# Kernel tuning notes

Hardware: AMD Instinct MI355X
Metric: run time of the kernel (lower is better)

The kernel has to match this reference:

```python
import jax, jax.numpy as jnp
import numpy as np

NUM_HEADS = 12
SEQ_H = 32
SEQ_W = 32
D_HALF = 32
ROPE_BASE = 10000.0
LN_EPS = 1e-5


def build_rope_cache(seq_len, head_dim, base=ROPE_BASE):
    inv_freq = 1.0 / base ** (jnp.arange(0, head_dim, 2, dtype=jnp.float32) / head_dim)
    t = jnp.arange(seq_len, dtype=jnp.float32)
    freqs = jnp.outer(t, inv_freq)  # [seq_len, head_dim//2]
    cos = jnp.repeat(jnp.cos(freqs), 2, axis=-1)  # [seq_len, head_dim]
    sin = jnp.repeat(jnp.sin(freqs), 2, axis=-1)
    return cos, sin


def apply_rope(x, cos, sin):
    # x: [B,H,N,d_sub], cos/sin: [N,d_sub]
    x_even, x_odd = x[..., ::2], x[..., 1::2]
    x_rot = jnp.stack([-x_odd, x_even], axis=-1).reshape(x.shape)
    return x * cos[None, None] + x_rot * sin[None, None]


def setup_inputs() -> dict:
    key = jax.random.key(0)
    ks = jax.random.split(key, 3)
    B, N, D = 8, 1025, 768
    return {
        "x": jax.random.normal(ks[0], (B, N, D), dtype=jnp.float32),
        "ln_g": jnp.ones((D,), dtype=jnp.float32),
        "ln_b": jnp.zeros((D,), dtype=jnp.float32),
        "w_qkv": jax.random.normal(ks[1], (3 * D, D), dtype=jnp.float32) * 0.02,
        "w_proj": jax.random.normal(ks[2], (D, D), dtype=jnp.float32) * 0.02,
        "b_proj": jnp.zeros((D,), dtype=jnp.float32),
    }


def reference(x, ln_g, ln_b, w_qkv, w_proj, b_proj):
    B, N, D = x.shape
    H = NUM_HEADS
    hd = D // H
    d2 = D_HALF
    scale = hd ** -0.5

    # LayerNorm
    mu = jnp.mean(x, axis=-1, keepdims=True)
    var = jnp.mean(jnp.square(x - mu), axis=-1, keepdims=True)
    xn = (x - mu) * jax.lax.rsqrt(var + LN_EPS) * ln_g + ln_b

    # QKV projection (no bias)
    qkv = jnp.einsum("bnd,ed->bne", xn, w_qkv).reshape(B, N, 3, H, hd)
    qkv = jnp.transpose(qkv, (2, 0, 3, 1, 4))  # [3,B,H,N,hd]
    q, k, v = qkv[0], qkv[1], qkv[2]

    # 2D position ids (CLS token -> row 0, col 0)
    patch_lin = jnp.arange(N - 1)
    rows = patch_lin // SEQ_W
    cols = patch_lin % SEQ_W
    zero = jnp.zeros((1,), dtype=patch_lin.dtype)
    row_ids = jnp.concatenate([zero, rows])
    col_ids = jnp.concatenate([zero, cols])

    cos_row, sin_row = build_rope_cache(SEQ_H, d2)
    cos_col, sin_col = build_rope_cache(SEQ_W, d2)
    cos_r, sin_r = cos_row[row_ids], sin_row[row_ids]  # [N,d2]
    cos_c, sin_c = cos_col[col_ids], sin_col[col_ids]

    q = jnp.concatenate(
        [apply_rope(q[..., :d2], cos_r, sin_r), apply_rope(q[..., d2:], cos_c, sin_c)], axis=-1)
    k = jnp.concatenate(
        [apply_rope(k[..., :d2], cos_r, sin_r), apply_rope(k[..., d2:], cos_c, sin_c)], axis=-1)

    attn = jnp.einsum("bhqd,bhkd->bhqk", q, k) * scale
    attn = jax.nn.softmax(attn, axis=-1)
    out = jnp.einsum("bhqk,bhkd->bhqd", attn, v)  # [B,H,N,hd]
    out = jnp.transpose(out, (0, 2, 1, 3)).reshape(B, N, D)
    return jnp.einsum("bnd,ed->bne", out, w_proj) + b_proj
```

## Files before the change

kernel.cpp:

```cpp
#include <hip/hip_runtime.h>
#include <hip/hip_bf16.h>

typedef unsigned short u16;

#define B_      8
#define N_      1025
#define D_      768
#define H_      12
#define HD_     64
#define M_REAL  (B_ * N_)
#define M_PAD   8320
#define QKVC    (3 * D_)

typedef __attribute__((ext_vector_type(8))) short bf16x8;
typedef __attribute__((ext_vector_type(4))) float f32x4;

static __device__ __forceinline__ float bf2f(u16 u) {
    union { unsigned int i; float f; } v; v.i = ((unsigned int)u) << 16; return v.f;
}
static __device__ __forceinline__ u16 f2bf(float f) {
    union { float f; unsigned int i; } v; v.f = f;
    unsigned int x = v.i;
    return (u16)((x + 0x7fffu + ((x >> 16) & 1u)) >> 16);
}

static __device__ __forceinline__ void g2l16(const u16* g, u16* l) {
    __builtin_amdgcn_global_load_lds(
        (const __attribute__((address_space(1))) unsigned int*)g,
        (__attribute__((address_space(3))) unsigned int*)l, 16, 0, 0);
}

__global__ __launch_bounds__(256)
void f2b2_kernel(const float* __restrict__ a, u16* __restrict__ oa, int na,
                 const float* __restrict__ b, u16* __restrict__ ob)
{
    int i = (blockIdx.x * 256 + threadIdx.x) * 4;
    const float* src; u16* dst;
    if (i < na) { src = a + i; dst = oa + i; }
    else        { src = b + (i - na); dst = ob + (i - na); }
    float4 v = *(const float4*)src;
    dst[0] = f2bf(v.x); dst[1] = f2bf(v.y);
    dst[2] = f2bf(v.z); dst[3] = f2bf(v.w);
}

__global__ __launch_bounds__(256)
void ln_kernel(const float* __restrict__ x, const float* __restrict__ g,
               const float* __restrict__ bvec, u16* __restrict__ xn)
{
    const int row = blockIdx.x;
    const int tid = threadIdx.x;
    const float* xr = x + (size_t)row * D_;
    float v[3];
    float s = 0.f, ss = 0.f;
#pragma unroll
    for (int j = 0; j < 3; j++) {
        float val = xr[tid + j * 256];
        v[j] = val; s += val; ss += val * val;
    }
    __shared__ float r1[256], r2[256];
    r1[tid] = s; r2[tid] = ss; __syncthreads();
    for (int off = 128; off > 0; off >>= 1) {
        if (tid < off) { r1[tid] += r1[tid + off]; r2[tid] += r2[tid + off]; }
        __syncthreads();
    }
    const float mean = r1[0] * (1.0f / D_);
    const float var  = r2[0] * (1.0f / D_) - mean * mean;
    const float rs   = rsqrtf(var + 1e-5f);
    u16* outr = xn + (size_t)row * D_;
#pragma unroll
    for (int j = 0; j < 3; j++) {
        int c = tid + j * 256;
        outr[c] = f2bf((v[j] - mean) * rs * g[c] + bvec[c]);
    }
}

template <typename OutT, bool ROPE>
__global__ __launch_bounds__(256)
void gemm_bt(const u16* __restrict__ A, const u16* __restrict__ B,
             OutT* __restrict__ C, const float* __restrict__ bias,
             int M_real, int Ncols, int K,
             int BM, int BN, int gh, int gw, int PC)
{
    const int l   = blockIdx.x;
    const int xcd = l & 7;
    const int i0  = l >> 3;
    const int pr  = xcd / PC, pc = xcd % PC;
    const int bm  = pr * gh + (i0 % gh);
    const int bn  = pc * gw + (i0 / gh);
    if (bm >= BM || bn >= BN) return;

    __shared__ __align__(16) unsigned char smem[34816];
    u16* As0 = (u16*)smem;
    u16* Bs0 = (u16*)(smem + 8192);
    u16* As1 = (u16*)(smem + 16384);
    u16* Bs1 = (u16*)(smem + 24576);
    u16*   ep16 = (u16*)smem;
    float* ep32 = (float*)smem;

    const int tid  = threadIdx.x;
    const int wave = tid >> 6, lane = tid & 63;
    const int wm   = (wave >> 1) * 64, wn = (wave & 1) * 64;
    const int lrow = lane & 15, lq = lane >> 4;
    const int lrow4 = lane >> 2, lchunk = lane & 3;

    int ar0 = bm * 128 + wave * 16 + lrow4;       if (ar0 >= M_real) ar0 = M_real - 1;
    int ar1 = bm * 128 + (wave + 4) * 16 + lrow4; if (ar1 >= M_real) ar1 = M_real - 1;
    const u16* apg0 = A + (size_t)ar0 * K + lchunk * 8;
    const u16* apg1 = A + (size_t)ar1 * K + lchunk * 8;
    const u16* bpg0 = B + (size_t)(bn * 128 + wave * 16 + lrow4) * K + lchunk * 8;
    const u16* bpg1 = B + (size_t)(bn * 128 + (wave + 4) * 16 + lrow4) * K + lchunk * 8;
    u16* asl0 = As0 + wave * 512;       u16* asl1 = As0 + (wave + 4) * 512;
    u16* bsl0 = Bs0 + wave * 512;       u16* bsl1 = Bs0 + (wave + 4) * 512;
    const int bufoff = 8192;

    f32x4 acc[4][4];
#pragma unroll
    for (int i = 0; i < 4; i++)
#pragma unroll
        for (int j = 0; j < 4; j++)
            acc[i][j] = (f32x4){0.f, 0.f, 0.f, 0.f};

    g2l16(apg0, asl0); g2l16(apg1, asl1);
    g2l16(bpg0, bsl0); g2l16(bpg1, bsl1);

    const int kTiles = K / 32;
    for (int kt = 0; kt < kTiles; kt++) {
        const int cur = kt & 1;
        __syncthreads();
        if (kt + 1 < kTiles) {
            const int k1 = (kt + 1) * 32;
            const int no = (cur ^ 1) * bufoff;
            g2l16(apg0 + k1, asl0 + no); g2l16(apg1 + k1, asl1 + no);
            g2l16(bpg0 + k1, bsl0 + no); g2l16(bpg1 + k1, bsl1 + no);
        }
        const u16* Asr = As0 + cur * bufoff;
        const u16* Bsr = Bs0 + cur * bufoff;
        bf16x8 af[4], bfr[4];
#pragma unroll
        for (int i = 0; i < 4; i++) {
            af[i]  = *(const bf16x8*)&Asr[(wm + i * 16 + lrow) * 32 + lq * 8];
            bfr[i] = *(const bf16x8*)&Bsr[(wn + i * 16 + lrow) * 32 + lq * 8];
        }
#pragma unroll
        for (int i = 0; i < 4; i++)
#pragma unroll
            for (int j = 0; j < 4; j++)
                acc[i][j] = __builtin_amdgcn_mfma_f32_16x16x32_bf16(af[i], bfr[j], acc[i][j], 0, 0, 0);
    }
    __syncthreads();

    if constexpr (sizeof(OutT) == 2) {
#pragma unroll
        for (int j = 0; j < 4; j++) {
            int gcol = bn * 128 + wn + j * 16 + lrow;
            float bv = bias ? bias[gcol] : 0.f;
            int qk = gcol / D_;
            int dh = gcol & 63;
            int half = dh >> 5, ii = (dh & 31) >> 1;
            float sgn = (dh & 1) ? 1.f : -1.f;
            float invf = exp2f(-(float)ii * 0.8304820237218406f);
#pragma unroll
            for (int i = 0; i < 4; i++)
#pragma unroll
                for (int r = 0; r < 4; r++) {
                    int grow = bm * 128 + wm + i * 16 + lq * 4 + r;
                    float val = acc[i][j][r] + bv;
                    if constexpr (ROPE) {
                        if (qk < 2) {
                            float partner = __shfl_xor(val, 1);
                            int n = grow % N_;
                            int pl = n - 1;
                            int pos = (n == 0) ? 0 : (half ? (pl & 31) : (pl >> 5));
                            float ang = (float)pos * invf;
                            val = val * __cosf(ang) + sgn * partner * __sinf(ang);
                        }
                    }
                    ep16[(wm + i * 16 + lq * 4 + r) * 136 + wn + j * 16 + lrow] = f2bf(val);
                }
        }
        __syncthreads();
#pragma unroll
        for (int c = 0; c < 8; c++) {
            int idx = tid + c * 256;
            int row = idx >> 4, l16 = idx & 15;
            int grow = bm * 128 + row;
            if (grow < M_real)
                *(uint4*)((u16*)C + (size_t)grow * Ncols + bn * 128 + l16 * 8) =
                    *(const uint4*)&ep16[row * 136 + l16 * 8];
        }
    } else {
#pragma unroll
        for (int s = 0; s < 2; s++) {
            if (s) __syncthreads();
            if (wm == s * 64) {
#pragma unroll
                for (int j = 0; j < 4; j++) {
                    int gcol = bn * 128 + wn + j * 16 + lrow;
                    float bv = bias ? bias[gcol] : 0.f;
#pragma unroll
                    for (int i = 0; i < 4; i++)
#pragma unroll
                        for (int r = 0; r < 4; r++)
                            ep32[(i * 16 + lq * 4 + r) * 132 + wn + j * 16 + lrow] =
                                acc[i][j][r] + bv;
                }
            }
            __syncthreads();
#pragma unroll
            for (int c = 0; c < 8; c++) {
                int idx = tid + c * 256;
                int row = idx >> 5, l32 = idx & 31;
                int grow = bm * 128 + s * 64 + row;
                if (grow < M_real)
                    *(uint4*)((float*)C + (size_t)grow * Ncols + bn * 128 + l32 * 4) =
                        *(const uint4*)&ep32[row * 132 + l32 * 4];
            }
        }
    }
}

__global__ __launch_bounds__(256)
void attn_mfma(const u16* __restrict__ qkv, u16* __restrict__ out)
{
    __shared__ __align__(16) u16 Kt[64][72];
    __shared__ __align__(16) u16 Vt[64][72];
    __shared__ __align__(16) u16 Ps[4][32][72];

    const int l   = blockIdx.x;
    const int xcd = l & 7;
    const int j0  = l >> 3;
    const int bh  = xcd * 12 + j0 / 9;
    const int b  = bh / H_, h = bh % H_;
    const int q0 = (j0 % 9) * 128;
    const int tid  = threadIdx.x;
    const int wave = tid >> 6, lane = tid & 63;
    const int lm = lane & 15, lq = lane >> 4;
    const int qw = q0 + wave * 32;

    bf16x8 qf[2][2];
#pragma unroll
    for (int sq = 0; sq < 2; sq++) {
        int qrow = qw + sq * 16 + lm; if (qrow > N_ - 1) qrow = N_ - 1;
        const u16* qptr = qkv + (size_t)(b * N_ + qrow) * QKVC + h * HD_;
        bf16x8 t0 = *(const bf16x8*)(qptr + lq * 8);
        bf16x8 t1 = *(const bf16x8*)(qptr + 32 + lq * 8);
#pragma unroll
        for (int j = 0; j < 8; j++) {
            t0[j] = (short)f2bf(bf2f((u16)t0[j]) * 0.125f);
            t1[j] = (short)f2bf(bf2f((u16)t1[j]) * 0.125f);
        }
        qf[sq][0] = t0; qf[sq][1] = t1;
    }

    float l_r[2][4];
    f32x4 o_acc[2][4];
#pragma unroll
    for (int sq = 0; sq < 2; sq++)
#pragma unroll
        for (int t = 0; t < 4; t++) {
            l_r[sq][t] = 0.f;
            o_acc[sq][t] = (f32x4){0.f, 0.f, 0.f, 0.f};
        }

    bf16x8 kreg[2], vreg[2];
    {
        int krow = lane; if (krow > N_ - 1) krow = N_ - 1;
        const u16* kvp = qkv + (size_t)(b * N_ + krow) * QKVC + h * HD_;
#pragma unroll
        for (int p = 0; p < 2; p++) {
            int dg = wave + p * 4;
            kreg[p] = *(const bf16x8*)(kvp + D_ + dg * 8);
            vreg[p] = *(const bf16x8*)(kvp + 2 * D_ + dg * 8);
        }
    }

    const int kTiles = (N_ + 63) / 64;
    for (int kt = 0; kt < kTiles; kt++) {
        const int kbase = kt * 64;
        __syncthreads();
#pragma unroll
        for (int p = 0; p < 2; p++) {
            int dg = wave + p * 4;
            *(bf16x8*)&Kt[lane][dg * 8] = kreg[p];
#pragma unroll
            for (int j = 0; j < 8; j++) Vt[dg * 8 + j][lane] = (u16)vreg[p][j];
        }
        __syncthreads();

        if (kt + 1 < kTiles) {
            int krow = kbase + 64 + lane; if (krow > N_ - 1) krow = N_ - 1;
            const u16* kvp = qkv + (size_t)(b * N_ + krow) * QKVC + h * HD_;
#pragma unroll
            for (int p = 0; p < 2; p++) {
                int dg = wave + p * 4;
                kreg[p] = *(const bf16x8*)(kvp + D_ + dg * 8);
                vreg[p] = *(const bf16x8*)(kvp + 2 * D_ + dg * 8);
            }
        }

        f32x4 sc[2][4];
#pragma unroll
        for (int st = 0; st < 4; st++) {
            bf16x8 kf0 = *(const bf16x8*)&Kt[st * 16 + lm][lq * 8];
            bf16x8 kf1 = *(const bf16x8*)&Kt[st * 16 + lm][32 + lq * 8];
#pragma unroll
            for (int sq = 0; sq < 2; sq++) {
                f32x4 s4 = (f32x4){0.f, 0.f, 0.f, 0.f};
                s4 = __builtin_amdgcn_mfma_f32_16x16x32_bf16(qf[sq][0], kf0, s4, 0, 0, 0);
                s4 = __builtin_amdgcn_mfma_f32_16x16x32_bf16(qf[sq][1], kf1, s4, 0, 0, 0);
                sc[sq][st] = s4;
            }
        }

#pragma unroll
        for (int st = 0; st < 4; st++) {
            bool ok = (kbase + st * 16 + lm) < N_;
#pragma unroll
            for (int sq = 0; sq < 2; sq++)
#pragma unroll
                for (int r = 0; r < 4; r++) {
                    float p = ok ? __expf(sc[sq][st][r]) : 0.f;
                    l_r[sq][r] += p;
                    Ps[wave][sq * 16 + lq * 4 + r][st * 16 + lm] = f2bf(p);
                }
        }
        asm volatile("s_waitcnt lgkmcnt(0)" ::: "memory");

        bf16x8 pa[2][2];
#pragma unroll
        for (int sq = 0; sq < 2; sq++) {
            pa[sq][0] = *(const bf16x8*)&Ps[wave][sq * 16 + lm][lq * 8];
            pa[sq][1] = *(const bf16x8*)&Ps[wave][sq * 16 + lm][32 + lq * 8];
        }
#pragma unroll
        for (int nt = 0; nt < 4; nt++) {
            bf16x8 vb0 = *(const bf16x8*)&Vt[nt * 16 + lm][lq * 8];
            bf16x8 vb1 = *(const bf16x8*)&Vt[nt * 16 + lm][32 + lq * 8];
#pragma unroll
            for (int sq = 0; sq < 2; sq++) {
                o_acc[sq][nt] = __builtin_amdgcn_mfma_f32_16x16x32_bf16(pa[sq][0], vb0, o_acc[sq][nt], 0, 0, 0);
                o_acc[sq][nt] = __builtin_amdgcn_mfma_f32_16x16x32_bf16(pa[sq][1], vb1, o_acc[sq][nt], 0, 0, 0);
            }
        }
    }

#pragma unroll
    for (int sq = 0; sq < 2; sq++)
#pragma unroll
        for (int r = 0; r < 4; r++) {
            float l2 = l_r[sq][r];
            l2 += __shfl_xor(l2, 1);
            l2 += __shfl_xor(l2, 2);
            l2 += __shfl_xor(l2, 4);
            l2 += __shfl_xor(l2, 8);
            int q = qw + sq * 16 + lq * 4 + r;
            if (q < N_) {
                float inv = 1.0f / l2;
                u16* orow = out + (size_t)(b * N_ + q) * D_ + h * HD_ + lm;
#pragma unroll
                for (int nt = 0; nt < 4; nt++)
                    orow[nt * 16] = f2bf(o_acc[sq][nt][r] * inv);
            }
        }
}

extern "C" void kernel_launch(void* const* d_in, const int* in_sizes, int n_in,
                              void* d_out, int out_size, void* d_ws, size_t ws_size,
                              hipStream_t stream)
{
    const float* x      = (const float*)d_in[0];
    const float* ln_g   = (const float*)d_in[1];
    const float* ln_b   = (const float*)d_in[2];
    const float* w_qkv  = (const float*)d_in[3];
    const float* w_proj = (const float*)d_in[4];
    const float* b_proj = (const float*)d_in[5];

    u16* wqkv_b  = (u16*)d_ws;
    u16* wproj_b = wqkv_b + (size_t)QKVC * D_;
    u16* xn      = wproj_b + (size_t)D_ * D_;
    u16* qkv     = xn + (size_t)M_PAD * D_;
    u16* attno   = xn;

    f2b2_kernel<<<(QKVC * D_ + D_ * D_) / 1024, 256, 0, stream>>>(
        w_qkv, wqkv_b, QKVC * D_, w_proj, wproj_b);

    ln_kernel<<<M_REAL, 256, 0, stream>>>(x, ln_g, ln_b, xn);

    gemm_bt<u16, true><<<1224, 256, 0, stream>>>(
        xn, wqkv_b, qkv, nullptr, M_REAL, QKVC, D_,
        65, 18, 17, 9, 2);

    attn_mfma<<<864, 256, 0, stream>>>(qkv, attno);

    gemm_bt<float, false><<<432, 256, 0, stream>>>(
        attno, wproj_b, (float*)d_out, b_proj, M_REAL, D_, D_,
        65, 6, 9, 6, 1);
}
```

Before: 231.8 us.

## Load K fragments directly from global and transpose score MFMA for packed P stores

Result: slower. 275.3 us (+18.7%).

```diff
diff --git a/kernel.cpp b/kernel.cpp
--- a/kernel.cpp
+++ b/kernel.cpp
@@ -22,6 +22,9 @@
     union { float f; unsigned int i; } v; v.f = f;
     unsigned int x = v.i;
     return (u16)((x + 0x7fffu + ((x >> 16) & 1u)) >> 16);
+}
+static __device__ __forceinline__ unsigned int fbits(float f) {
+    union { float f; unsigned int i; } v; v.f = f; return v.i;
 }
 
 static __device__ __forceinline__ void g2l16(const u16* g, u16* l) {
@@ -92,8 +95,6 @@
     __shared__ __align__(16) unsigned char smem[34816];
     u16* As0 = (u16*)smem;
     u16* Bs0 = (u16*)(smem + 8192);
-    u16* As1 = (u16*)(smem + 16384);
-    u16* Bs1 = (u16*)(smem + 24576);
     u16*   ep16 = (u16*)smem;
     float* ep32 = (float*)smem;
 
@@ -222,9 +223,9 @@
 __global__ __launch_bounds__(256)
 void attn_mfma(const u16* __restrict__ qkv, u16* __restrict__ out)
 {
-    __shared__ __align__(16) u16 Kt[64][72];
     __shared__ __align__(16) u16 Vt[64][72];
     __shared__ __align__(16) u16 Ps[4][32][72];
+    __shared__ float Lw[4][32];
 
     const int l   = blockIdx.x;
     const int xcd = l & 7;
@@ -252,26 +253,21 @@
         qf[sq][0] = t0; qf[sq][1] = t1;
     }
 
-    float l_r[2][4];
+    float l_r[2] = {0.f, 0.f};
     f32x4 o_acc[2][4];
 #pragma unroll
     for (int sq = 0; sq < 2; sq++)
 #pragma unroll
-        for (int t = 0; t < 4; t++) {
-            l_r[sq][t] = 0.f;
+        for (int t = 0; t < 4; t++)
             o_acc[sq][t] = (f32x4){0.f, 0.f, 0.f, 0.f};
-        }
-
-    bf16x8 kreg[2], vreg[2];
+
+    bf16x8 vreg[2];
     {
         int krow = lane; if (krow > N_ - 1) krow = N_ - 1;
-        const u16* kvp = qkv + (size_t)(b * N_ + krow) * QKVC + h * HD_;
-#pragma unroll
-        for (int p = 0; p < 2; p++) {
-            int dg = wave + p * 4;
-            kreg[p] = *(const bf16x8*)(kvp + D_ + dg * 8);
-            vreg[p] = *(const bf16x8*)(kvp + 2 * D_ + dg * 8);
-        }
+        const u16* kvp = qkv + (size_t)(b * N_ + krow) * QKVC + h * HD_ + 2 * D_;
+#pragma unroll
+        for (int p = 0; p < 2; p++)
+            vreg[p] = *(const bf16x8*)(kvp + (wave + p * 4) * 8);
     }
 
     const int kTiles = (N_ + 63) / 64;
@@ -281,7 +277,6 @@
 #pragma unroll
         for (int p = 0; p < 2; p++) {
             int dg = wave + p * 4;
-            *(bf16x8*)&Kt[lane][dg * 8] = kreg[p];
 #pragma unroll
             for (int j = 0; j < 8; j++) Vt[dg * 8 + j][lane] = (u16)vreg[p][j];
         }
@@ -289,40 +284,45 @@
 
         if (kt + 1 < kTiles) {
             int krow = kbase + 64 + lane; if (krow > N_ - 1) krow = N_ - 1;
-            const u16* kvp = qkv + (size_t)(b * N_ + krow) * QKVC + h * HD_;
-#pragma unroll
-            for (int p = 0; p < 2; p++) {
-                int dg = wave + p * 4;
-                kreg[p] = *(const bf16x8*)(kvp + D_ + dg * 8);
-                vreg[p] = *(const bf16x8*)(kvp + 2 * D_ + dg * 8);
-            }
+            const u16* kvp = qkv + (size_t)(b * N_ + krow) * QKVC + h * HD_ + 2 * D_;
+#pragma unroll
+            for (int p = 0; p < 2; p++)
+                vreg[p] = *(const bf16x8*)(kvp + (wave + p * 4) * 8);
         }
 
         f32x4 sc[2][4];
 #pragma unroll
         for (int st = 0; st < 4; st++) {
-            bf16x8 kf0 = *(const bf16x8*)&Kt[st * 16 + lm][lq * 8];
-            bf16x8 kf1 = *(const bf16x8*)&Kt[st * 16 + lm][32 + lq * 8];
+            int krow = kbase + st * 16 + lm; if (krow > N_ - 1) krow = N_ - 1;
+            const u16* kp = qkv + (size_t)(b * N_ + krow) * QKVC + h * HD_ + D_;
+            bf16x8 kf0 = *(const bf16x8*)(kp + lq * 8);
+            bf16x8 kf1 = *(const bf16x8*)(kp + 32 + lq * 8);
 #pragma unroll
             for (int sq = 0; sq < 2; sq++) {
                 f32x4 s4 = (f32x4){0.f, 0.f, 0.f, 0.f};
-                s4 = __builtin_amdgcn_mfma_f32_16x16x32_bf16(qf[sq][0], kf0, s4, 0, 0, 0);
-                s4 = __builtin_amdgcn_mfma_f32_16x16x32_bf16(qf[sq][1], kf1, s4, 0, 0, 0);
+                s4 = __builtin_amdgcn_mfma_f32_16x16x32_bf16(kf0, qf[sq][0], s4, 0, 0, 0);
+                s4 = __builtin_amdgcn_mfma_f32_16x16x32_bf16(kf1, qf[sq][1], s4, 0, 0, 0);
                 sc[sq][st] = s4;
             }
         }
 
 #pragma unroll
         for (int st = 0; st < 4; st++) {
-            bool ok = (kbase + st * 16 + lm) < N_;
-#pragma unroll
-            for (int sq = 0; sq < 2; sq++)
+            int keyb = kbase + st * 16 + lq * 4;
+#pragma unroll
+            for (int sq = 0; sq < 2; sq++) {
+                unsigned int u[4];
 #pragma unroll
                 for (int r = 0; r < 4; r++) {
-                    float p = ok ? __expf(sc[sq][st][r]) : 0.f;
-                    l_r[sq][r] += p;
-                    Ps[wave][sq * 16 + lq * 4 + r][st * 16 + lm] = f2bf(p);
+                    float p = (keyb + r < N_) ? __expf(sc[sq][st][r]) : 0.f;
+                    l_r[sq] += p;
+                    u[r] = fbits(p) + 0x8000u;
                 }
+                uint2 pk;
+                pk.x = (u[0] >> 16) | (u[1] & 0xffff0000u);
+                pk.y = (u[2] >> 16) | (u[3] & 0xffff0000u);
+                *(uint2*)&Ps[wave][sq * 16 + lm][st * 16 + lq * 4] = pk;
+            }
         }
         asm volatile("s_waitcnt lgkmcnt(0)" ::: "memory");
 
@@ -345,17 +345,21 @@
     }
 
 #pragma unroll
+    for (int sq = 0; sq < 2; sq++) {
+        float l2 = l_r[sq];
+        l2 += __shfl_xor(l2, 16);
+        l2 += __shfl_xor(l2, 32);
+        if (lq == 0) Lw[wave][sq * 16 + lm] = l2;
+    }
+    asm volatile("s_waitcnt lgkmcnt(0)" ::: "memory");
+
+#pragma unroll
     for (int sq = 0; sq < 2; sq++)
 #pragma unroll
         for (int r = 0; r < 4; r++) {
-            float l2 = l_r[sq][r];
-            l2 += __shfl_xor(l2, 1);
-            l2 += __shfl_xor(l2, 2);
-            l2 += __shfl_xor(l2, 4);
-            l2 += __shfl_xor(l2, 8);
             int q = qw + sq * 16 + lq * 4 + r;
             if (q < N_) {
-                float inv = 1.0f / l2;
+                float inv = 1.0f / Lw[wave][sq * 16 + lq * 4 + r];
                 u16* orow = out + (size_t)(b * N_ + q) * D_ + h * HD_ + lm;
 #pragma unroll
                 for (int nt = 0; nt < 4; nt++)
```
